# Kernel tuning notes

Measured on AMD Instinct MI355X. Metric: run time of the kernel, lower is better.

The kernel has to match this reference:

```python
import jax, jax.numpy as jnp
import numpy as np

NF, NV = 200000, 100000
C_IN, MULT, K = 128, 2, 16
C_OUT = 128
BN_EPS = 1e-3


def setup_inputs() -> dict:
    key = jax.random.key(0)
    ks = jax.random.split(key, 8)
    inputs = jax.random.normal(ks[0], (NF, C_IN), dtype=jnp.float32)
    filt_coeff = jax.random.uniform(ks[1], (NF, K), dtype=jnp.float32)
    face = jax.random.randint(ks[2], (NF, 3), 0, NV, dtype=jnp.int32)
    nf_count = jax.random.randint(ks[3], (NV,), 0, 12, dtype=jnp.int32)
    vt_map = jnp.arange(NV, dtype=jnp.int32)
    # parameters (xavier-normal-like init for weights)
    sw_std = float(np.sqrt(2.0 / (C_IN + MULT)))
    spatial_weights = jax.random.normal(ks[4], (K, C_IN, MULT), dtype=jnp.float32) * sw_std
    dw_std = float(np.sqrt(2.0 / (C_IN * MULT + C_OUT)))
    depth_weights = jax.random.normal(ks[5], (C_IN * MULT, C_OUT), dtype=jnp.float32) * dw_std
    biases = jnp.zeros((1, C_OUT), dtype=jnp.float32)
    gamma = jnp.ones((C_OUT,), dtype=jnp.float32)
    beta = jnp.zeros((C_OUT,), dtype=jnp.float32)
    return {"inputs": inputs, "filt_coeff": filt_coeff, "face": face,
            "nf_count": nf_count, "vt_map": vt_map,
            "spatial_weights": spatial_weights, "depth_weights": depth_weights,
            "biases": biases, "gamma": gamma, "beta": beta}


def reference(inputs, filt_coeff, face, nf_count, vt_map,
              spatial_weights, depth_weights, biases, gamma, beta):
    Nf, C = inputs.shape
    Kb, _, M = spatial_weights.shape
    Nv = nf_count.shape[0]
    # per-face mixture kernel:  w[f,c,m] = sum_k filt_coeff[f,k] * spatial_weights[k,c,m]
    w = jnp.einsum('fk,kcm->fcm', filt_coeff, spatial_weights)
    feat = (inputs[:, :, None] * w).reshape(Nf, C * M)  # [Nf, C*M]
    # scatter facet features to the 3 incident vertices (mapped via vt_map)
    tgt = vt_map[face]  # [Nf, 3]
    agg = jnp.zeros((Nv, C * M), dtype=feat.dtype)
    for j in range(3):  # small fixed structural loop (3 verts per triangle)
        agg = agg + jax.ops.segment_sum(feat, tgt[:, j], num_segments=Nv)
    denom = jnp.maximum(nf_count, 1).astype(feat.dtype)[:, None]
    vert = agg / denom  # mean over incident facets, [Nv, C*M]
    # dense depthwise (pointwise) matmul + bias + ReLU
    out = vert @ depth_weights + biases
    out = jax.nn.relu(out)
    # BatchNorm1d (training-mode batch statistics, eps=1e-3)
    mean = out.mean(axis=0)
    var = out.var(axis=0)
    out = (out - mean) * jax.lax.rsqrt(var + BN_EPS) * gamma + beta
    return out
```

## Files before the change

kernel.cpp:

```cpp
#include <hip/hip_runtime.h>
#include <hip/hip_bf16.h>


constexpr int C_IN  = 128;
constexpr int KF    = 16;
constexpr int CM    = 256;
constexpr int C_OUT = 128;
constexpr int CAP   = 32;
constexpr int GB    = 1024;
constexpr int FT    = 64;
constexpr int GRIDF = 512;
constexpr float BN_EPS = 1e-3f;

typedef __attribute__((ext_vector_type(8))) short short8;
typedef __attribute__((ext_vector_type(4))) float f32x4;

__device__ __forceinline__ ushort f2bf(float x) {
  union { float f; unsigned u; } v; v.f = x;
  return (ushort)((v.u + 0x7fffu + ((v.u >> 16) & 1u)) >> 16);
}
__device__ __forceinline__ float b2f(ushort u) {
  return __uint_as_float((unsigned)u << 16);
}
__device__ __forceinline__ uint pk2(float a, float b) {
  __hip_bfloat162 h = __float22bfloat162_rn(float2{a, b});
  return *(uint*)&h;
}
__device__ __forceinline__ void dma16(const float* g, void* l) {
  __builtin_amdgcn_global_load_lds(
      (const __attribute__((address_space(1))) void*)g,
      (__attribute__((address_space(3))) void*)l, 16, 0, 0);
}
__device__ __forceinline__ void bar_raw() {
  __builtin_amdgcn_s_barrier();
  asm volatile("" ::: "memory");
}
__device__ __forceinline__ void bar_lds() {
  asm volatile("s_waitcnt lgkmcnt(0)" ::: "memory");
  __builtin_amdgcn_s_barrier();
  asm volatile("" ::: "memory");
}

__global__ __launch_bounds__(256) void k_prepfill(
    const float* __restrict__ dw, const float* __restrict__ sw,
    ushort* __restrict__ dwt, ushort* __restrict__ swt,
    const int* __restrict__ face, const int* __restrict__ vt_map,
    int* __restrict__ cnt, int* __restrict__ slots, int n_inc) {
  const int b = blockIdx.x, tid = threadIdx.x;
  if (b < 64) {
    int i = b * 512 + tid;
#pragma unroll
    for (int r = 0; r < 2; ++r, i += 256) {
      int n = i >> 8, k = i & 255;
      dwt[i] = f2bf(dw[k * C_OUT + n]);
    }
  } else if (b < 96) {
    int i = (b - 64) * 256 + tid;
    int cm = i >> 5, k = i & 31;
    swt[i] = (k < KF) ? f2bf(sw[k * CM + cm]) : (ushort)0;
  } else {
    int i = (b - 96) * 256 + tid;
    if (i < n_inc) {
      int f = i / 3;
      int v = vt_map[face[i]];
      int p = atomicAdd(&cnt[v], 1);
      if (p < CAP) slots[(size_t)v * CAP + p] = f;
    }
  }
}

__global__ __launch_bounds__(256, 2) void k_faceg(
    const float* __restrict__ inp, const float* __restrict__ fc,
    const ushort* __restrict__ swt, const ushort* __restrict__ dwt,
    ushort* __restrict__ g, int ntiles) {
  __shared__ __align__(1024) ushort s_buf[2][FT * 256];

  const int tid  = threadIdx.x;
  const int w    = tid >> 6;
  const int lane = tid & 63;
  const int rm   = lane & 15;
  const int kg   = lane >> 4;

  short8 a1[4];
#pragma unroll
  for (int ct = 0; ct < 4; ++ct)
    a1[ct] = *(const short8*)&swt[(size_t)(w * 64 + ct * 16 + rm) * 32 + kg * 8];
  short8 bfr[2][8];
#pragma unroll
  for (int nt = 0; nt < 2; ++nt) {
    const int n = (w * 2 + nt) * 16 + rm;
#pragma unroll
    for (int ks = 0; ks < 8; ++ks)
      bfr[nt][ks] = *(const short8*)&dwt[n * 256 + ks * 32 + kg * 8];
  }

  auto issue_dma = [&](int buf, int fb) {
#pragma unroll
    for (int it = 0; it < 8; ++it) {
      const int row   = w * 16 + it * 2 + (lane >> 5);
      const int chunk = lane & 31;
      const float* src = inp + (size_t)(fb + row) * C_IN + ((chunk ^ (row & 7)) << 2);
      dma16(src, (char*)s_buf + buf * 32768 + w * 8192 + it * 1024);
    }
  };

  int t = blockIdx.x;
  issue_dma(0, t * FT);
  int cur = 0;

  for (; t < ntiles; t += GRIDF, cur ^= 1) {
    const int fb = t * FT;
    char* sb = (char*)s_buf + cur * 32768;

    bar_lds();

    float4 p0[4], p1[4];
#pragma unroll
    for (int ft = 0; ft < 4; ++ft) {
      const float* fr = &fc[(size_t)(fb + ft * 16 + rm) * KF + (kg & 1) * 8];
      p0[ft] = *(const float4*)fr;
      p1[ft] = *(const float4*)(fr + 4);
    }

    const int tn = t + GRIDF;
    if (tn < ntiles) {
      issue_dma(cur ^ 1, tn * FT);
      asm volatile("s_waitcnt vmcnt(8)" ::: "memory");
    } else {
      asm volatile("s_waitcnt vmcnt(0)" ::: "memory");
    }

    short8 b1[4];
#pragma unroll
    for (int ft = 0; ft < 4; ++ft) {
      uint4 u;
      u.x = pk2(p0[ft].x, p0[ft].y); u.y = pk2(p0[ft].z, p0[ft].w);
      u.z = pk2(p1[ft].x, p1[ft].y); u.w = pk2(p1[ft].z, p1[ft].w);
      if (kg >= 2) u = uint4{0, 0, 0, 0};
      b1[ft] = *(short8*)&u;
    }

    bar_raw();

#pragma unroll
    for (int ft = 0; ft < 4; ++ft) {
#pragma unroll
      for (int ct = 0; ct < 4; ++ct) {
        f32x4 acc = {0.f, 0.f, 0.f, 0.f};
        acc = __builtin_amdgcn_mfma_f32_16x16x32_bf16(a1[ct], b1[ft], acc, 0, 0, 0);
        const int face = ft * 16 + rm;
        const int cmb  = w * 64 + ct * 16 + kg * 4;
        const int byt  = face * 512 + ((((cmb * 2) >> 4) ^ (face & 7)) << 4)
                       + ((cmb * 2) & 15);
        const float2 ivv = *(const float2*)(sb + byt);
        uint2 pw;
        pw.x = pk2(acc[0] * ivv.x, acc[1] * ivv.x);
        pw.y = pk2(acc[2] * ivv.y, acc[3] * ivv.y);
        *(uint2*)(sb + byt) = pw;
      }
    }

    bar_lds();

    f32x4 acc2[4][2];
#pragma unroll
    for (int fs = 0; fs < 4; ++fs)
#pragma unroll
      for (int nt = 0; nt < 2; ++nt)
        acc2[fs][nt] = (f32x4){0.f, 0.f, 0.f, 0.f};

#pragma unroll
    for (int fs = 0; fs < 4; ++fs)
#pragma unroll
      for (int ks = 0; ks < 8; ++ks) {
        const int row = fs * 16 + rm;
        const int byt = row * 512 + (((ks * 4 + kg) ^ (row & 7)) << 4);
        const short8 af = *(const short8*)(sb + byt);
        acc2[fs][0] = __builtin_amdgcn_mfma_f32_16x16x32_bf16(bfr[0][ks], af, acc2[fs][0], 0, 0, 0);
        acc2[fs][1] = __builtin_amdgcn_mfma_f32_16x16x32_bf16(bfr[1][ks], af, acc2[fs][1], 0, 0, 0);
      }

#pragma unroll
    for (int fs = 0; fs < 4; ++fs) {
      const size_t rowoff = (size_t)(fb + fs * 16 + rm) * C_OUT;
#pragma unroll
      for (int nt = 0; nt < 2; ++nt) {
        uint2 pw;
        pw.x = pk2(acc2[fs][nt][0], acc2[fs][nt][1]);
        pw.y = pk2(acc2[fs][nt][2], acc2[fs][nt][3]);
        *(uint2*)&g[rowoff + (w * 2 + nt) * 16 + kg * 4] = pw;
      }
    }
  }
}

__global__ __launch_bounds__(256) void k_gather(
    const ushort* __restrict__ g, const int* __restrict__ cnt,
    const int* __restrict__ slots, const int* __restrict__ nf_cnt,
    const float* __restrict__ bias, ushort* __restrict__ pre,
    float* __restrict__ part, int nv, int ntiles) {
  __shared__ float s_red[256][8];

  const int tid = threadIdx.x;
  const int q   = tid & 15;
  const int vg  = tid >> 4;
  const int c8  = q * 8;

  float bs[8];
#pragma unroll
  for (int j = 0; j < 8; ++j) bs[j] = bias[c8 + j];
  float st_s[8], st_q[8];
#pragma unroll
  for (int j = 0; j < 8; ++j) { st_s[j] = 0.f; st_q[j] = 0.f; }

  for (int tile = blockIdx.x; tile < ntiles; tile += gridDim.x) {
    const int v = tile * 16 + vg;
    int deg = cnt[v]; deg = deg > CAP ? CAP : deg;
    const int* sl = &slots[(size_t)v * CAP];

    float a[8];
#pragma unroll
    for (int j = 0; j < 8; ++j) a[j] = 0.f;

    int t = 0;
    for (; t + 4 <= deg; t += 4) {
      const int4 ff = *(const int4*)&sl[t];
      const short8 r0 = *(const short8*)&g[(size_t)ff.x * C_OUT + c8];
      const short8 r1 = *(const short8*)&g[(size_t)ff.y * C_OUT + c8];
      const short8 r2 = *(const short8*)&g[(size_t)ff.z * C_OUT + c8];
      const short8 r3 = *(const short8*)&g[(size_t)ff.w * C_OUT + c8];
#pragma unroll
      for (int j = 0; j < 8; ++j)
        a[j] += (b2f((ushort)r0[j]) + b2f((ushort)r1[j]))
              + (b2f((ushort)r2[j]) + b2f((ushort)r3[j]));
    }
    for (; t < deg; ++t) {
      const short8 r0 = *(const short8*)&g[(size_t)sl[t] * C_OUT + c8];
#pragma unroll
      for (int j = 0; j < 8; ++j) a[j] += b2f((ushort)r0[j]);
    }

    int d = nf_cnt[v]; if (d < 1) d = 1;
    const float inv = 1.0f / (float)d;
    float r[8];
#pragma unroll
    for (int j = 0; j < 8; ++j) {
      r[j] = fmaxf(fmaf(a[j], inv, bs[j]), 0.f);
      st_s[j] += r[j];
      st_q[j] = fmaf(r[j], r[j], st_q[j]);
    }
    uint4 u;
    u.x = pk2(r[0], r[1]); u.y = pk2(r[2], r[3]);
    u.z = pk2(r[4], r[5]); u.w = pk2(r[6], r[7]);
    *(short8*)&pre[(size_t)v * C_OUT + c8] = *(short8*)&u;
  }

#pragma unroll
  for (int j = 0; j < 8; ++j) s_red[tid][j] = st_s[j];
  __syncthreads();
  if (tid < 16) {
    for (int j = 0; j < 8; ++j) {
      float x = 0.f;
      for (int gg = 0; gg < 16; ++gg) x += s_red[gg * 16 + tid][j];
      part[(size_t)(tid * 8 + j) * GB + blockIdx.x] = x;
    }
  }
  __syncthreads();
#pragma unroll
  for (int j = 0; j < 8; ++j) s_red[tid][j] = st_q[j];
  __syncthreads();
  if (tid < 16) {
    for (int j = 0; j < 8; ++j) {
      float x = 0.f;
      for (int gg = 0; gg < 16; ++gg) x += s_red[gg * 16 + tid][j];
      part[(size_t)(128 + tid * 8 + j) * GB + blockIdx.x] = x;
    }
  }
}

__global__ __launch_bounds__(256) void k_red(const float* __restrict__ part,
                                             float* __restrict__ red) {
  const int j   = blockIdx.x;
  const int tid = threadIdx.x;
  float v = 0.f;
#pragma unroll
  for (int b = 0; b < GB; b += 256) v += part[(size_t)j * GB + b + tid];
#pragma unroll
  for (int off = 32; off > 0; off >>= 1) v += __shfl_down(v, off);
  __shared__ float sred[4];
  if ((tid & 63) == 0) sred[tid >> 6] = v;
  __syncthreads();
  if (tid == 0) red[j] = sred[0] + sred[1] + sred[2] + sred[3];
}

__global__ void k_fin(const float* __restrict__ red,
                      const float* __restrict__ gamma, const float* __restrict__ beta,
                      float* __restrict__ scale, float* __restrict__ shift, float invN) {
  int o = threadIdx.x;
  float mean = red[o] * invN;
  float var  = red[128 + o] * invN - mean * mean;
  float sc   = gamma[o] * rsqrtf(var + BN_EPS);
  scale[o] = sc;
  shift[o] = fmaf(-mean, sc, beta[o]);
}

__global__ __launch_bounds__(256) void k_bn(const ushort* __restrict__ pre,
                                            const float* __restrict__ scale,
                                            const float* __restrict__ shift,
                                            float* __restrict__ out, int n8) {
  int idx = blockIdx.x * blockDim.x + threadIdx.x;
  const int stride = gridDim.x * blockDim.x;
  for (; idx < n8; idx += stride) {
    const short8 pv = *(const short8*)&pre[(size_t)idx * 8];
    const int base = (idx * 8) & (C_OUT - 1);
    const float4 sc0 = *(const float4*)&scale[base];
    const float4 sc1 = *(const float4*)&scale[base + 4];
    const float4 sh0 = *(const float4*)&shift[base];
    const float4 sh1 = *(const float4*)&shift[base + 4];
    float4 o0, o1;
    o0.x = fmaf(b2f((ushort)pv[0]), sc0.x, sh0.x);
    o0.y = fmaf(b2f((ushort)pv[1]), sc0.y, sh0.y);
    o0.z = fmaf(b2f((ushort)pv[2]), sc0.z, sh0.z);
    o0.w = fmaf(b2f((ushort)pv[3]), sc0.w, sh0.w);
    o1.x = fmaf(b2f((ushort)pv[4]), sc1.x, sh1.x);
    o1.y = fmaf(b2f((ushort)pv[5]), sc1.y, sh1.y);
    o1.z = fmaf(b2f((ushort)pv[6]), sc1.z, sh1.z);
    o1.w = fmaf(b2f((ushort)pv[7]), sc1.w, sh1.w);
    *(float4*)&out[(size_t)idx * 8]     = o0;
    *(float4*)&out[(size_t)idx * 8 + 4] = o1;
  }
}

extern "C" void kernel_launch(void* const* d_in, const int* in_sizes, int n_in,
                              void* d_out, int out_size, void* d_ws, size_t ws_size,
                              hipStream_t stream) {
  const float* inputs = (const float*)d_in[0];
  const float* fc     = (const float*)d_in[1];
  const int*   face   = (const int*)d_in[2];
  const int*   nf_cnt = (const int*)d_in[3];
  const int*   vt_map = (const int*)d_in[4];
  const float* sw     = (const float*)d_in[5];
  const float* dw     = (const float*)d_in[6];
  const float* bias   = (const float*)d_in[7];
  const float* gamma  = (const float*)d_in[8];
  const float* beta   = (const float*)d_in[9];
  float* out = (float*)d_out;

  const int nf = in_sizes[0] / C_IN;
  const int nv = in_sizes[3];

  char* p = (char*)d_ws;
  int*    cnt   = (int*)p;            p += (size_t)nv * 4;
  float*  scale = (float*)p;          p += C_OUT * 4;
  float*  shift = (float*)p;          p += C_OUT * 4;
  float*  red   = (float*)p;          p += 256 * 4;
  float*  part  = (float*)p;          p += (size_t)256 * GB * 4;
  ushort* dwt   = (ushort*)p;         p += (size_t)C_OUT * CM * 2;
  ushort* swt   = (ushort*)p;         p += (size_t)CM * 32 * 2;
  int*    slots = (int*)p;            p += (size_t)nv * CAP * 4;
  ushort* g     = (ushort*)p;         p += (size_t)nf * C_OUT * 2;
  ushort* pre   = (ushort*)p;

  hipMemsetAsync(cnt, 0, (size_t)nv * 4, stream);

  const int n_inc = nf * 3;
  const int fill_blocks = (n_inc + 255) / 256;
  k_prepfill<<<96 + fill_blocks, 256, 0, stream>>>(dw, sw, dwt, swt,
                                                   face, vt_map, cnt, slots, n_inc);

  const int ntiles_f = (nf + FT - 1) / FT;
  k_faceg<<<GRIDF, 256, 0, stream>>>(inputs, fc, swt, dwt, g, ntiles_f);

  const int ntiles_v = (nv + 15) / 16;
  k_gather<<<GB, 256, 0, stream>>>(g, cnt, slots, nf_cnt, bias, pre, part, nv, ntiles_v);

  k_red<<<256, 256, 0, stream>>>(part, red);
  k_fin<<<1, 128, 0, stream>>>(red, gamma, beta, scale, shift, 1.0f / (float)nv);

  const int n8 = (nv * C_OUT) / 8;
  k_bn<<<2048, 256, 0, stream>>>(pre, scale, shift, out, n8);
}
```

Baseline: 137.1 us.

## Load inputs directly to registers, drop LDS double buffer, raise occupancy

Replaces the double-buffered global-to-LDS DMA pipeline for the input features with direct per-thread float2 register loads, and keeps a single LDS buffer. This halves shared memory per block, so launch bounds and grid size can go from 2 to 3 blocks per CU (grid 512 to 768). The aim is to hide load latency through more resident waves instead of explicit prefetch. In exchange it loses the cross-iteration overlap of the next tile's loads and issues less coalesced strided global reads.

```diff
diff --git a/kernel.cpp b/kernel.cpp
--- a/kernel.cpp
+++ b/kernel.cpp
@@ -9,7 +9,7 @@
 constexpr int CAP   = 32;
 constexpr int GB    = 1024;
 constexpr int FT    = 64;
-constexpr int GRIDF = 512;
+constexpr int GRIDF = 768;
 constexpr float BN_EPS = 1e-3f;
 
 typedef __attribute__((ext_vector_type(8))) short short8;
@@ -25,15 +25,6 @@
 __device__ __forceinline__ uint pk2(float a, float b) {
   __hip_bfloat162 h = __float22bfloat162_rn(float2{a, b});
   return *(uint*)&h;
-}
-__device__ __forceinline__ void dma16(const float* g, void* l) {
-  __builtin_amdgcn_global_load_lds(
-      (const __attribute__((address_space(1))) void*)g,
-      (__attribute__((address_space(3))) void*)l, 16, 0, 0);
-}
-__device__ __forceinline__ void bar_raw() {
-  __builtin_amdgcn_s_barrier();
-  asm volatile("" ::: "memory");
 }
 __device__ __forceinline__ void bar_lds() {
   asm volatile("s_waitcnt lgkmcnt(0)" ::: "memory");
@@ -69,11 +60,12 @@
   }
 }
 
-__global__ __launch_bounds__(256, 2) void k_faceg(
+__global__ __launch_bounds__(256, 3) void k_faceg(
     const float* __restrict__ inp, const float* __restrict__ fc,
     const ushort* __restrict__ swt, const ushort* __restrict__ dwt,
     ushort* __restrict__ g, int ntiles) {
-  __shared__ __align__(1024) ushort s_buf[2][FT * 256];
+  __shared__ __align__(1024) ushort s_feat[FT * 256];
+  char* sb = (char*)s_feat;
 
   const int tid  = threadIdx.x;
   const int w    = tid >> 6;
@@ -94,26 +86,17 @@
       bfr[nt][ks] = *(const short8*)&dwt[n * 256 + ks * 32 + kg * 8];
   }
 
-  auto issue_dma = [&](int buf, int fb) {
-#pragma unroll
-    for (int it = 0; it < 8; ++it) {
-      const int row   = w * 16 + it * 2 + (lane >> 5);
-      const int chunk = lane & 31;
-      const float* src = inp + (size_t)(fb + row) * C_IN + ((chunk ^ (row & 7)) << 2);
-      dma16(src, (char*)s_buf + buf * 32768 + w * 8192 + it * 1024);
-    }
-  };
-
-  int t = blockIdx.x;
-  issue_dma(0, t * FT);
-  int cur = 0;
-
-  for (; t < ntiles; t += GRIDF, cur ^= 1) {
+  for (int t = blockIdx.x; t < ntiles; t += GRIDF) {
     const int fb = t * FT;
-    char* sb = (char*)s_buf + cur * 32768;
-
-    bar_lds();
-
+
+    float2 iv[4][4];
+#pragma unroll
+    for (int ft = 0; ft < 4; ++ft) {
+      const float* rowp = &inp[(size_t)(fb + ft * 16 + rm) * C_IN];
+#pragma unroll
+      for (int ct = 0; ct < 4; ++ct)
+        iv[ft][ct] = *(const float2*)&rowp[(w * 16 + ct * 4 + kg) * 2];
+    }
     float4 p0[4], p1[4];
 #pragma unroll
     for (int ft = 0; ft < 4; ++ft) {
@@ -121,14 +104,9 @@
       p0[ft] = *(const float4*)fr;
       p1[ft] = *(const float4*)(fr + 4);
     }
-
-    const int tn = t + GRIDF;
-    if (tn < ntiles) {
-      issue_dma(cur ^ 1, tn * FT);
-      asm volatile("s_waitcnt vmcnt(8)" ::: "memory");
-    } else {
-      asm volatile("s_waitcnt vmcnt(0)" ::: "memory");
-    }
+    __builtin_amdgcn_sched_barrier(0);
+
+    bar_lds();
 
     short8 b1[4];
 #pragma unroll
@@ -139,8 +117,6 @@
       if (kg >= 2) u = uint4{0, 0, 0, 0};
       b1[ft] = *(short8*)&u;
     }
-
-    bar_raw();
 
 #pragma unroll
     for (int ft = 0; ft < 4; ++ft) {
@@ -152,10 +128,11 @@
         const int cmb  = w * 64 + ct * 16 + kg * 4;
         const int byt  = face * 512 + ((((cmb * 2) >> 4) ^ (face & 7)) << 4)
                        + ((cmb * 2) & 15);
-        const float2 ivv = *(const float2*)(sb + byt);
+        const float i0 = iv[ft][ct].x;
+        const float i1 = iv[ft][ct].y;
         uint2 pw;
-        pw.x = pk2(acc[0] * ivv.x, acc[1] * ivv.x);
-        pw.y = pk2(acc[2] * ivv.y, acc[3] * ivv.y);
+        pw.x = pk2(acc[0] * i0, acc[1] * i0);
+        pw.y = pk2(acc[2] * i1, acc[3] * i1);
         *(uint2*)(sb + byt) = pw;
       }
     }
```

Result: slower. 155.4 us (+13.3%).
